# Kernel optimization log

Measured on AMD Instinct MI355X. Metric: run time of the kernel, lower is better.

Reference implementation:

```python
import jax, jax.numpy as jnp
import numpy as np

B, S, E = 4, 2048, 1024
H = 16
D = E // H  # head_dim = 64


def setup_inputs() -> dict:
    key = jax.random.key(0)
    ks = jax.random.split(key, 7)
    query = jax.random.normal(ks[0], (B, S, E), dtype=jnp.float32)
    k_in = jax.random.normal(ks[1], (B, S, E), dtype=jnp.float32)
    v_in = jax.random.normal(ks[2], (B, S, E), dtype=jnp.float32)
    lim_qkv = 1.0 / np.sqrt(E)
    W_qkv = jax.random.uniform(ks[3], (E, 3 * E), jnp.float32, -lim_qkv, lim_qkv)
    b_qkv = jax.random.uniform(ks[4], (3 * E,), jnp.float32, -lim_qkv, lim_qkv)
    W_out = jax.random.uniform(ks[5], (E, E), jnp.float32, -lim_qkv, lim_qkv)
    b_out = jax.random.uniform(ks[6], (E,), jnp.float32, -lim_qkv, lim_qkv)
    return {"query": query, "key": k_in, "value": v_in,
            "W_qkv": W_qkv, "b_qkv": b_qkv, "W_out": W_out, "b_out": b_out}


def reference(query, key, value, W_qkv, b_qkv, W_out, b_out):
    # NOTE: original module ignores key/value; q,k,v all derived from query.
    b, s, e = query.shape
    qkv = query @ W_qkv + b_qkv                     # [B,S,3E]
    qkv = qkv.reshape(b, s, 3, H, D)
    q, k, v = qkv[:, :, 0], qkv[:, :, 1], qkv[:, :, 2]   # [B,S,H,D]
    scale = jnp.sqrt(jnp.asarray(D, dtype=jnp.float32))
    scores = jnp.einsum('bqhd,bkhd->bhqk', q, k) / scale  # [B,H,S,S]
    attn = jax.nn.softmax(scores, axis=-1)
    out = jnp.einsum('bhqk,bkhd->bqhd', attn, v).reshape(b, s, e)
    return out @ W_out + b_out
```

## Files before the change

kernel.cpp:

```cpp
#include <hip/hip_runtime.h>
#include <hip/hip_bf16.h>

#define Bc 4
#define Sc 2048
#define Ec 1024
#define Hc 16
#define Dc 64

typedef __bf16 bf16_t;
typedef __bf16 bf16x4 __attribute__((ext_vector_type(4)));
typedef __bf16 bf16x8 __attribute__((ext_vector_type(8)));
typedef float f32x4 __attribute__((ext_vector_type(4)));

extern "C" __device__ float __ocml_native_exp2_f32(float);

__device__ __forceinline__ f32x4 mfma16(bf16x8 a, bf16x8 b, f32x4 c) {
    return __builtin_amdgcn_mfma_f32_16x16x32_bf16(a, b, c, 0, 0, 0);
}

__device__ __forceinline__ void gload16(const bf16_t* g, bf16_t* l) {
    __builtin_amdgcn_global_load_lds(
        (const __attribute__((address_space(1))) unsigned int*)g,
        (__attribute__((address_space(3))) unsigned int*)l, 16, 0, 0);
}

#define FENCE asm volatile("" ::: "memory")
#define BARRIER do { FENCE; __builtin_amdgcn_s_barrier(); FENCE; } while (0)

__global__ __launch_bounds__(256)
void cvt_bf16(const float* __restrict__ in, bf16_t* __restrict__ out, int n4)
{
    int i = blockIdx.x * 256 + threadIdx.x;
    if (i >= n4) return;
    float4 v = ((const float4*)in)[i];
    alignas(8) bf16_t o[4];
    o[0] = (bf16_t)v.x; o[1] = (bf16_t)v.y; o[2] = (bf16_t)v.z; o[3] = (bf16_t)v.w;
    ((uint2*)out)[i] = *(uint2*)o;
}

__global__ __launch_bounds__(256)
void transpose_w(const float* __restrict__ W, bf16_t* __restrict__ Wt, int K, int N)
{
    __shared__ float T[64][65];
    const int kt = blockIdx.y, nt = blockIdx.x;
    const int r = threadIdx.x >> 4;
    const int c = (threadIdx.x & 15) * 4;
    #pragma unroll
    for (int p = 0; p < 4; p++) {
        float4 v = *(const float4*)(W + (size_t)(kt*64 + r + p*16)*N + nt*64 + c);
        T[r + p*16][c] = v.x; T[r + p*16][c+1] = v.y;
        T[r + p*16][c+2] = v.z; T[r + p*16][c+3] = v.w;
    }
    __syncthreads();
    #pragma unroll
    for (int p = 0; p < 4; p++) {
        int n = nt*64 + r + p*16;
        alignas(8) bf16_t tmp[4];
        #pragma unroll
        for (int j = 0; j < 4; j++) tmp[j] = (bf16_t)T[c + j][r + p*16];
        *(uint2*)(Wt + (size_t)n*K + kt*64 + c) = *(uint2*)tmp;
    }
}

__global__ __launch_bounds__(256)
void transpose_v(const bf16_t* __restrict__ qkv, bf16_t* __restrict__ vt)
{
    __shared__ bf16_t T[64][72];
    const int bh = blockIdx.y, st = blockIdx.x;
    const int b = bh >> 4, h = bh & 15;
    const int sr = threadIdx.x >> 3;
    const int dc = (threadIdx.x & 7) * 8;
    #pragma unroll
    for (int p = 0; p < 2; p++) {
        const bf16_t* src = qkv + (size_t)(b*Sc + st*64 + sr + p*32)*(3*Ec) + 2*Ec + h*Dc + dc;
        *(uint4*)&T[sr + p*32][dc] = *(const uint4*)src;
    }
    __syncthreads();
    const int dr = threadIdx.x >> 3;
    const int sc2 = (threadIdx.x & 7) * 8;
    #pragma unroll
    for (int p = 0; p < 2; p++) {
        alignas(16) bf16_t tmp[8];
        #pragma unroll
        for (int j = 0; j < 8; j++)
            tmp[j] = T[sc2 + j][dr + p*32];
        *(uint4*)(vt + (size_t)bh*Dc*Sc + (size_t)(dr + p*32)*Sc + st*64 + sc2) = *(uint4*)tmp;
    }
}

template<int OUT_IS_F32>
__global__ __launch_bounds__(512)
void gemm3b(const bf16_t* __restrict__ A, const bf16_t* __restrict__ Bt,
            const float* __restrict__ biasp, void* __restrict__ Cp,
            int M, int N, int K)
{
    __shared__ bf16_t LS[3][384*64];

    const int tid  = threadIdx.x;
    const int wave = tid >> 6;
    const int lane = tid & 63;
    const int quad = lane >> 4;
    const int l16  = lane & 15;
    const int wm   = (wave >> 2) * 64;
    const int wn   = (wave & 3) * 64;

    const int nwg = gridDim.x * gridDim.y;
    const int bid = blockIdx.y * gridDim.x + blockIdx.x;
    const int cpx = nwg >> 3;
    const int swz = (bid & 7) * cpx + (bid >> 3);
    const int nbx = N >> 8;
    const int m0  = (swz / nbx) * 128;
    const int n0  = (swz % nbx) * 256;

    const int NT = K >> 6;

    const int srow = lane >> 3;
    const int sch  = (lane & 7) ^ ((wave*4 + (lane >> 4)) & 7);
    const bf16_t* aSrc = A  + (size_t)(m0 + wave*8 + srow)*K + sch*8;
    const bf16_t* bSrc = Bt + (size_t)(n0 + wave*8 + srow)*K + sch*8;

    const int fsw = (l16 >> 1) & 7;

    f32x4 acc[4][4] = {};

    auto stage = [&](int bi, int t) {
        const bf16_t* ap = aSrc + t*64;
        const bf16_t* bp = bSrc + t*64;
        gload16(ap,               &LS[bi][(0         + wave*8)*64]);
        gload16(ap + (size_t)64*K, &LS[bi][(64        + wave*8)*64]);
        gload16(bp,               &LS[bi][(128 +   0 + wave*8)*64]);
        gload16(bp + (size_t)64*K, &LS[bi][(128 +  64 + wave*8)*64]);
        gload16(bp + (size_t)128*K,&LS[bi][(128 + 128 + wave*8)*64]);
        gload16(bp + (size_t)192*K,&LS[bi][(128 + 192 + wave*8)*64]);
    };

    stage(0, 0);
    stage(1, 1);
    asm volatile("s_waitcnt vmcnt(6)" ::: "memory");
    BARRIER;

    int bi = 0;
    for (int t = 0; t < NT; ++t) {
        bf16x8 af[4][2], bfr[4][2];
        #pragma unroll
        for (int mi = 0; mi < 4; mi++)
            #pragma unroll
            for (int kk = 0; kk < 2; kk++)
                af[mi][kk] = *(const bf16x8*)
                    &LS[bi][(wm + mi*16 + l16)*64 + ((kk*4+quad)^fsw)*8];
        #pragma unroll
        for (int ni = 0; ni < 4; ni++)
            #pragma unroll
            for (int kk = 0; kk < 2; kk++)
                bfr[ni][kk] = *(const bf16x8*)
                    &LS[bi][(128 + wn + ni*16 + l16)*64 + ((kk*4+quad)^fsw)*8];

        if (t + 2 < NT) {
            int b2 = bi + 2; if (b2 >= 3) b2 -= 3;
            stage(b2, t + 2);
        }
        BARRIER;
        asm volatile("s_waitcnt lgkmcnt(0)" ::: "memory");
        __builtin_amdgcn_sched_barrier(0);
        __builtin_amdgcn_s_setprio(1);
        #pragma unroll
        for (int mi = 0; mi < 4; mi++)
            #pragma unroll
            for (int ni = 0; ni < 4; ni++)
                #pragma unroll
                for (int kk = 0; kk < 2; kk++)
                    acc[mi][ni] = mfma16(af[mi][kk], bfr[ni][kk], acc[mi][ni]);
        __builtin_amdgcn_s_setprio(0);
        if (t + 2 < NT)      asm volatile("s_waitcnt vmcnt(6)" ::: "memory");
        else if (t + 1 < NT) asm volatile("s_waitcnt vmcnt(0)" ::: "memory");
        BARRIER;
        bi = bi + 1; if (bi >= 3) bi = 0;
    }

    float bv[4];
    #pragma unroll
    for (int ni = 0; ni < 4; ni++) bv[ni] = biasp[n0 + wn + ni*16 + l16];

    #pragma unroll
    for (int mi = 0; mi < 4; mi++)
        #pragma unroll
        for (int ni = 0; ni < 4; ni++)
            #pragma unroll
            for (int r = 0; r < 4; r++) {
                int row = m0 + wm + mi*16 + quad*4 + r;
                int col = n0 + wn + ni*16 + l16;
                float v = acc[mi][ni][r] + bv[ni];
                if (OUT_IS_F32) ((float*)Cp)[(size_t)row * N + col] = v;
                else            ((bf16_t*)Cp)[(size_t)row * N + col] = (bf16_t)v;
            }
}

__global__ __launch_bounds__(256, 2)
void attn12(const bf16_t* __restrict__ qkv, const bf16_t* __restrict__ vt,
            bf16_t* __restrict__ aout)
{
    __shared__ bf16_t Ks[64][72];
    __shared__ bf16_t Vs[64][72];
    __shared__ bf16_t Po[4][16][72];

    const int tid  = threadIdx.x;
    const int wave = tid >> 6;
    const int lane = tid & 63;
    const int quad = lane >> 4;
    const int l16  = lane & 15;
    const int bh   = blockIdx.x;
    const int b    = bh >> 4;
    const int h    = bh & 15;
    const int qt   = blockIdx.y;
    const float kscale = 0.125f * 1.44269504088896340736f;

    bf16x8 qf[4][2];
    #pragma unroll
    for (int qi = 0; qi < 4; qi++) {
        const bf16_t* qrow = qkv + (size_t)(b*Sc + qt*256 + wave*64 + qi*16 + l16)*(3*Ec) + h*Dc;
        qf[qi][0] = *(const bf16x8*)(qrow + quad*8);
        qf[qi][1] = *(const bf16x8*)(qrow + 32 + quad*8);
        #pragma unroll
        for (int f = 0; f < 2; f++)
            #pragma unroll
            for (int e = 0; e < 8; e++)
                qf[qi][f][e] = (bf16_t)((float)qf[qi][f][e] * kscale);
    }

    f32x4 acc[4][4] = {};
    float lpart[4] = {};

    const int krw   = tid >> 2;
    const int dbase = (tid & 3) * 16;

    const bf16_t* kbase = qkv + (size_t)(b*Sc + krw)*(3*Ec) + Ec + h*Dc + dbase;
    const bf16_t* vbase = vt + (size_t)bh*Dc*Sc + (size_t)krw*Sc + dbase;
    const size_t kstep = (size_t)64 * (3*Ec);
    uint4 ku0 = ((const uint4*)kbase)[0];
    uint4 ku1 = ((const uint4*)kbase)[1];
    uint4 vu0 = ((const uint4*)vbase)[0];
    uint4 vu1 = ((const uint4*)vbase)[1];

    for (int kt = 0; kt < Sc/64; kt++) {
        __syncthreads();
        *(uint4*)&Ks[krw][dbase]     = ku0;
        *(uint4*)&Ks[krw][dbase + 8] = ku1;
        *(uint4*)&Vs[krw][dbase]     = vu0;
        *(uint4*)&Vs[krw][dbase + 8] = vu1;
        __syncthreads();

        if (kt < Sc/64 - 1) {
            const bf16_t* kn = kbase + (size_t)(kt+1) * kstep;
            const bf16_t* vn = vbase + (kt+1) * 64;
            ku0 = ((const uint4*)kn)[0];
            ku1 = ((const uint4*)kn)[1];
            vu0 = ((const uint4*)vn)[0];
            vu1 = ((const uint4*)vn)[1];
        }

        bf16x8 kf[4][2];
        #pragma unroll
        for (int ki = 0; ki < 4; ki++) {
            kf[ki][0] = *(const bf16x8*)&Ks[ki*16 + l16][quad*8];
            kf[ki][1] = *(const bf16x8*)&Ks[ki*16 + l16][32 + quad*8];
        }

        bf16x4 pp[4][4];
        #pragma unroll
        for (int ki = 0; ki < 4; ki++) {
            #pragma unroll
            for (int qi = 0; qi < 4; qi++) {
                f32x4 z = {};
                z = mfma16(kf[ki][0], qf[qi][0], z);
                z = mfma16(kf[ki][1], qf[qi][1], z);
                float p0 = __ocml_native_exp2_f32(z[0]);
                float p1 = __ocml_native_exp2_f32(z[1]);
                float p2 = __ocml_native_exp2_f32(z[2]);
                float p3 = __ocml_native_exp2_f32(z[3]);
                lpart[qi] += (p0 + p1) + (p2 + p3);
                bf16x4 w;
                w[0] = (bf16_t)p0; w[1] = (bf16_t)p1;
                w[2] = (bf16_t)p2; w[3] = (bf16_t)p3;
                pp[ki][qi] = w;
            }
        }

        #pragma unroll
        for (int c = 0; c < 2; c++) {
            bf16x8 pcat[4];
            #pragma unroll
            for (int qi = 0; qi < 4; qi++)
                pcat[qi] = __builtin_shufflevector(pp[2*c][qi], pp[2*c+1][qi],
                                                   0,1,2,3,4,5,6,7);
            #pragma unroll
            for (int di = 0; di < 4; di++) {
                bf16x4 v0 = *(const bf16x4*)&Vs[di*16 + l16][c*32 + 4*quad];
                bf16x4 v1 = *(const bf16x4*)&Vs[di*16 + l16][c*32 + 16 + 4*quad];
                bf16x8 vf = __builtin_shufflevector(v0, v1, 0,1,2,3,4,5,6,7);
                #pragma unroll
                for (int qi = 0; qi < 4; qi++)
                    acc[di][qi] = mfma16(vf, pcat[qi], acc[di][qi]);
            }
        }
    }

    float inv[4];
    #pragma unroll
    for (int qi = 0; qi < 4; qi++) {
        float l = lpart[qi];
        l += __shfl_xor(l, 16);
        l += __shfl_xor(l, 32);
        inv[qi] = 1.0f / l;
    }

    const int qrd  = lane >> 2;
    const int dch  = (lane & 3) * 16;
    #pragma unroll
    for (int qi = 0; qi < 4; qi++) {
        #pragma unroll
        for (int di = 0; di < 4; di++) {
            alignas(8) bf16_t w[4];
            #pragma unroll
            for (int r = 0; r < 4; r++)
                w[r] = (bf16_t)(acc[di][qi][r] * inv[qi]);
            *(uint2*)&Po[wave][l16][di*16 + quad*4] = *(uint2*)w;
        }
        asm volatile("s_waitcnt lgkmcnt(0)" ::: "memory");
        uint4 o0 = *(const uint4*)&Po[wave][qrd][dch];
        uint4 o1 = *(const uint4*)&Po[wave][qrd][dch + 8];
        bf16_t* dst = aout + (size_t)(b*Sc + qt*256 + wave*64 + qi*16 + qrd)*Ec + h*Dc + dch;
        ((uint4*)dst)[0] = o0;
        ((uint4*)dst)[1] = o1;
    }
}

extern "C" void kernel_launch(void* const* d_in, const int* in_sizes, int n_in,
                              void* d_out, int out_size, void* d_ws, size_t ws_size,
                              hipStream_t stream) {
    const float* query = (const float*)d_in[0];
    const float* W_qkv = (const float*)d_in[3];
    const float* b_qkv = (const float*)d_in[4];
    const float* W_out = (const float*)d_in[5];
    const float* b_out = (const float*)d_in[6];
    float* out = (float*)d_out;

    const size_t MT = (size_t)Bc * Sc;
    char* ws = (char*)d_ws;
    size_t off = 0;
    bf16_t* qbf    = (bf16_t*)(ws + off); off += MT*Ec*2;
    bf16_t* qkv_ws = (bf16_t*)(ws + off); off += MT*3*Ec*2;
    bf16_t* vt_ws  = (bf16_t*)(ws + off); off += MT*Ec*2;
    bf16_t* wqkv_t = (bf16_t*)(ws + off); off += (size_t)3*Ec*Ec*2;
    bf16_t* wout_t = (bf16_t*)(ws + off); off += (size_t)Ec*Ec*2;

    cvt_bf16<<<(MT*Ec/4 + 255)/256, 256, 0, stream>>>(query, qbf, (int)(MT*Ec/4));
    transpose_w<<<dim3(3*Ec/64, Ec/64), 256, 0, stream>>>(W_qkv, wqkv_t, Ec, 3*Ec);
    transpose_w<<<dim3(Ec/64, Ec/64), 256, 0, stream>>>(W_out, wout_t, Ec, Ec);

    gemm3b<0><<<dim3(3*Ec/256, MT/128), 512, 0, stream>>>(
        qbf, wqkv_t, b_qkv, qkv_ws, (int)MT, 3*Ec, Ec);

    transpose_v<<<dim3(Sc/64, Bc*Hc), 256, 0, stream>>>(qkv_ws, vt_ws);

    attn12<<<dim3(Bc*Hc, Sc/256), 256, 0, stream>>>(qkv_ws, vt_ws, qbf);

    gemm3b<1><<<dim3(Ec/256, MT/128), 512, 0, stream>>>(
        qbf, wout_t, b_out, out, (int)MT, Ec, Ec);
}
```

Baseline: 303.9 us.

## Fuse prep kernels and write transposed V directly from QKV GEMM epilogue

Merges the query conversion and the two weight transposes into one launch, which removes two kernel launches. The V-column tiles of the QKV GEMM now transpose through LDS in the epilogue and write the V^T layout directly, so the separate transpose_v kernel and its extra read/write pass over V are gone. In exchange the GEMM epilogue gains a branch and an LDS round-trip for the V tiles, and those tiles no longer write V into the qkv buffer.

```diff
diff --git a/kernel.cpp b/kernel.cpp
--- a/kernel.cpp
+++ b/kernel.cpp
@@ -28,21 +28,27 @@
 #define BARRIER do { FENCE; __builtin_amdgcn_s_barrier(); FENCE; } while (0)
 
 __global__ __launch_bounds__(256)
-void cvt_bf16(const float* __restrict__ in, bf16_t* __restrict__ out, int n4)
-{
-    int i = blockIdx.x * 256 + threadIdx.x;
-    if (i >= n4) return;
-    float4 v = ((const float4*)in)[i];
-    alignas(8) bf16_t o[4];
-    o[0] = (bf16_t)v.x; o[1] = (bf16_t)v.y; o[2] = (bf16_t)v.z; o[3] = (bf16_t)v.w;
-    ((uint2*)out)[i] = *(uint2*)o;
-}
-
-__global__ __launch_bounds__(256)
-void transpose_w(const float* __restrict__ W, bf16_t* __restrict__ Wt, int K, int N)
+void prep(const float* __restrict__ query, bf16_t* __restrict__ qbf,
+          const float* __restrict__ W_qkv, bf16_t* __restrict__ wqkv_t,
+          const float* __restrict__ W_out, bf16_t* __restrict__ wout_t,
+          int n4)
 {
     __shared__ float T[64][65];
-    const int kt = blockIdx.y, nt = blockIdx.x;
+    const int blk = blockIdx.x;
+    if (blk < 8192) {
+        int i = blk * 256 + threadIdx.x;
+        if (i < n4) {
+            float4 v = ((const float4*)query)[i];
+            alignas(8) bf16_t o[4];
+            o[0] = (bf16_t)v.x; o[1] = (bf16_t)v.y;
+            o[2] = (bf16_t)v.z; o[3] = (bf16_t)v.w;
+            ((uint2*)qbf)[i] = *(uint2*)o;
+        }
+        return;
+    }
+    const float* W; bf16_t* Wt; int K, N, kt, nt;
+    if (blk < 8192 + 768) { int id = blk - 8192; W = W_qkv; Wt = wqkv_t; K = Ec; N = 3*Ec; nt = id % 48; kt = id / 48; }
+    else                  { int id = blk - 8960; W = W_out; Wt = wout_t; K = Ec; N = Ec;   nt = id % 16; kt = id / 16; }
     const int r = threadIdx.x >> 4;
     const int c = (threadIdx.x & 15) * 4;
     #pragma unroll
@@ -62,37 +68,11 @@
     }
 }
 
-__global__ __launch_bounds__(256)
-void transpose_v(const bf16_t* __restrict__ qkv, bf16_t* __restrict__ vt)
-{
-    __shared__ bf16_t T[64][72];
-    const int bh = blockIdx.y, st = blockIdx.x;
-    const int b = bh >> 4, h = bh & 15;
-    const int sr = threadIdx.x >> 3;
-    const int dc = (threadIdx.x & 7) * 8;
-    #pragma unroll
-    for (int p = 0; p < 2; p++) {
-        const bf16_t* src = qkv + (size_t)(b*Sc + st*64 + sr + p*32)*(3*Ec) + 2*Ec + h*Dc + dc;
-        *(uint4*)&T[sr + p*32][dc] = *(const uint4*)src;
-    }
-    __syncthreads();
-    const int dr = threadIdx.x >> 3;
-    const int sc2 = (threadIdx.x & 7) * 8;
-    #pragma unroll
-    for (int p = 0; p < 2; p++) {
-        alignas(16) bf16_t tmp[8];
-        #pragma unroll
-        for (int j = 0; j < 8; j++)
-            tmp[j] = T[sc2 + j][dr + p*32];
-        *(uint4*)(vt + (size_t)bh*Dc*Sc + (size_t)(dr + p*32)*Sc + st*64 + sc2) = *(uint4*)tmp;
-    }
-}
-
 template<int OUT_IS_F32>
 __global__ __launch_bounds__(512)
 void gemm3b(const bf16_t* __restrict__ A, const bf16_t* __restrict__ Bt,
             const float* __restrict__ biasp, void* __restrict__ Cp,
-            int M, int N, int K)
+            int M, int N, int K, bf16_t* __restrict__ vtp)
 {
     __shared__ bf16_t LS[3][384*64];
 
@@ -180,6 +160,39 @@
     float bv[4];
     #pragma unroll
     for (int ni = 0; ni < 4; ni++) bv[ni] = biasp[n0 + wn + ni*16 + l16];
+
+    if (!OUT_IS_F32 && vtp && n0 >= 2*Ec) {
+        bf16_t* T = &LS[0][0];
+        #pragma unroll
+        for (int mi = 0; mi < 4; mi++)
+            #pragma unroll
+            for (int ni = 0; ni < 4; ni++) {
+                const int cl = wn + ni*16 + l16;
+                const int sb = wm + mi*16 + quad*4;
+                alignas(8) bf16_t w[4];
+                #pragma unroll
+                for (int r = 0; r < 4; r++)
+                    w[r] = (bf16_t)(acc[mi][ni][r] + bv[ni]);
+                *(uint2*)&T[cl*136 + sb] = *(uint2*)w;
+            }
+        __syncthreads();
+        const int b   = m0 >> 11;
+        const int sr0 = m0 & (Sc - 1);
+        const int h0  = (n0 - 2*Ec) >> 6;
+        const int s0  = (tid & 7) * 16;
+        #pragma unroll
+        for (int cb = 0; cb < 4; cb++) {
+            const int cl = cb*64 + (tid >> 3);
+            const int bh = b*Hc + h0 + (cl >> 6);
+            const int d  = cl & 63;
+            bf16_t* dst = vtp + ((size_t)bh*Dc + d)*Sc + sr0 + s0;
+            uint4 v0 = *(const uint4*)&T[cl*136 + s0];
+            uint4 v1 = *(const uint4*)&T[cl*136 + s0 + 8];
+            ((uint4*)dst)[0] = v0;
+            ((uint4*)dst)[1] = v1;
+        }
+        return;
+    }
 
     #pragma unroll
     for (int mi = 0; mi < 4; mi++)
@@ -353,17 +366,14 @@
     bf16_t* wqkv_t = (bf16_t*)(ws + off); off += (size_t)3*Ec*Ec*2;
     bf16_t* wout_t = (bf16_t*)(ws + off); off += (size_t)Ec*Ec*2;
 
-    cvt_bf16<<<(MT*Ec/4 + 255)/256, 256, 0, stream>>>(query, qbf, (int)(MT*Ec/4));
-    transpose_w<<<dim3(3*Ec/64, Ec/64), 256, 0, stream>>>(W_qkv, wqkv_t, Ec, 3*Ec);
-    transpose_w<<<dim3(Ec/64, Ec/64), 256, 0, stream>>>(W_out, wout_t, Ec, Ec);
+    prep<<<8192 + 768 + 256, 256, 0, stream>>>(
+        query, qbf, W_qkv, wqkv_t, W_out, wout_t, (int)(MT*Ec/4));
 
     gemm3b<0><<<dim3(3*Ec/256, MT/128), 512, 0, stream>>>(
-        qbf, wqkv_t, b_qkv, qkv_ws, (int)MT, 3*Ec, Ec);
-
-    transpose_v<<<dim3(Sc/64, Bc*Hc), 256, 0, stream>>>(qkv_ws, vt_ws);
+        qbf, wqkv_t, b_qkv, qkv_ws, (int)MT, 3*Ec, Ec, vt_ws);
 
     attn12<<<dim3(Bc*Hc, Sc/256), 256, 0, stream>>>(qkv_ws, vt_ws, qbf);
 
     gemm3b<1><<<dim3(Ec/256, MT/128), 512, 0, stream>>>(
-        qbf, wout_t, b_out, out, (int)MT, Ec, Ec);
-}
+        qbf, wout_t, b_out, out, (int)MT, Ec, Ec, nullptr);
+}
```

Result: faster. 297.8 us (-2.0%).
